# Kernel optimization log

Measured on AMD Instinct MI355X. Metric: run time of the kernel, lower is better.

Reference implementation:

```python
import jax, jax.numpy as jnp
import numpy as np

B, H, S, DK, DV = 2, 16, 2048, 64, 64


def setup_inputs() -> dict:
    key = jax.random.key(0)
    kq, kk, kv = jax.random.split(key, 3)
    Q = jax.random.normal(kq, (B, H, S, DK), dtype=jnp.float32)
    K = jax.random.normal(kk, (B, H, S, DK), dtype=jnp.float32)
    V = jax.random.normal(kv, (B, H, S, DV), dtype=jnp.float32)
    # causal mask: True = masked (upper triangle), broadcast to [B,H,S,S]
    causal = jnp.triu(jnp.ones((S, S), dtype=bool), k=1)
    attn_mask = jnp.broadcast_to(causal, (B, H, S, S))
    return {"Q": Q, "K": K, "V": V, "attn_mask": attn_mask}


def reference(Q, K, V, attn_mask):
    d_k = Q.shape[-1]
    # scores: [B,H,len_q,len_k]
    scores = jnp.einsum('bhqd,bhkd->bhqk', Q, K) / jnp.sqrt(jnp.float32(d_k))
    scores = jnp.where(attn_mask, -jnp.inf, scores)
    attn = jax.nn.softmax(scores, axis=-1)
    # context: [B,H,len_q,d_v]
    context = jnp.einsum('bhqk,bhkv->bhqv', attn, V)
    return context
```

## Files before the change

kernel.cpp:

```cpp
#include <hip/hip_runtime.h>
#include <hip/hip_bf16.h>
#include <math.h>

#define S_LEN 2048
#define DKV 64
#define NBH 32
#define QBLK 64
#define NQB (S_LEN / QBLK)
#define NKT (S_LEN / 64)
#define TILE_SH 4096

typedef __attribute__((ext_vector_type(8))) short bf16x8;
typedef __attribute__((ext_vector_type(16))) float f32x16;
typedef __attribute__((ext_vector_type(4))) float f32x4;
typedef __attribute__((ext_vector_type(4))) unsigned uint4v;

__device__ __forceinline__ short f2bf(float f) {
    union { float f; unsigned u; } x; x.f = f;
    unsigned r = (x.u + 0x7FFFu + ((x.u >> 16) & 1u)) >> 16;
    return (short)r;
}

__device__ __forceinline__ unsigned cvtpk(float lo, float hi) {
    unsigned r;
    asm("v_cvt_pk_bf16_f32 %0, %1, %2" : "=v"(r) : "v"(lo), "v"(hi));
    return r;
}

#define GLOAD_LDS16(g, s)                                                        \
    __builtin_amdgcn_global_load_lds(                                            \
        (const __attribute__((address_space(1))) unsigned*)(g),                  \
        (__attribute__((address_space(3))) unsigned*)(s), 16, 0, 0)

__global__ __launch_bounds__(256)
void prep_kv(const float* __restrict__ K, const float* __restrict__ V,
             short* __restrict__ wsK, short* __restrict__ wsV) {
    const int tile = blockIdx.x, bh = blockIdx.y, tid = threadIdx.x;
    const float* Kp = K + ((size_t)bh * S_LEN + tile * 64) * DKV;
    const float* Vp = V + ((size_t)bh * S_LEN + tile * 64) * DKV;
    short* outK = wsK + ((size_t)bh * NKT + tile) * TILE_SH;
    short* outV = wsV + ((size_t)bh * NKT + tile) * TILE_SH;

    __shared__ short Klds[64 * 64];
    __shared__ short Vl[64 * 64];

#pragma unroll
    for (int i = 0; i < 2; ++i) {
        const int chunk = i * 256 + tid;
        const int row = chunk >> 3, c8 = chunk & 7;
        const float* ksrc = Kp + row * DKV + c8 * 8;
        float4 a = *(const float4*)ksrc, b = *(const float4*)(ksrc + 4);
        uint4v tw;
        tw[0] = cvtpk(a.x, a.y); tw[1] = cvtpk(a.z, a.w);
        tw[2] = cvtpk(b.x, b.y); tw[3] = cvtpk(b.z, b.w);
        const int sidxK = (((c8 >> 1) * 2 + (row >> 5)) * 64) |
                          (((c8 & 1) << 5) | (row & 31));
        *(uint4v*)&Klds[sidxK * 8] = tw;

        const float* vs = Vp + row * DKV + c8 * 8;
        float4 c = *(const float4*)vs, d = *(const float4*)(vs + 4);
        uint4v uw;
        uw[0] = cvtpk(c.x, c.y); uw[1] = cvtpk(c.z, c.w);
        uw[2] = cvtpk(d.x, d.y); uw[3] = cvtpk(d.z, d.w);
        *(uint4v*)&Vl[chunk * 8] = uw;
    }
    __syncthreads();

#pragma unroll
    for (int i = 0; i < 2; ++i) {
        const int s = i * 256 + tid;
        *(bf16x8*)(outK + s * 8) = *(const bf16x8*)&Klds[s * 8];
        const int group = s >> 6;
        const int cc = group >> 1, th = group & 1;
        const int lane = s & 63;
        const int hh = lane >> 5, r31 = lane & 31;
        const int vd = 32 * th + r31;
        const int key0 = 16 * cc + 8 * hh;
        bf16x8 t;
#pragma unroll
        for (int j = 0; j < 8; ++j) t[j] = Vl[(key0 + j) * 64 + vd];
        *(bf16x8*)(outV + s * 8) = t;
    }
}

__global__ __launch_bounds__(256, 4)
void attn_fwd(const float* __restrict__ Q, const short* __restrict__ wsK,
              const short* __restrict__ wsV, float* __restrict__ O) {
    const int tid = threadIdx.x;
    const int l   = tid & 63;
    const int w   = tid >> 6;
    const int st  = w & 1;
    const int ks  = w >> 1;
    const int h   = l >> 5;
    const int q31 = l & 31;

    const int id = blockIdx.x;
    const int bh = ((id & 7) << 2) | ((id >> 3) & 3);
    const int r  = (id >> 5) & 7;
    const int qt = id >> 8;
    const int qb = (qt == 0) ? (31 - r) : (qt == 1) ? r
                 : (qt == 2) ? (23 - r) : (8 + r);

    __shared__ char smem[32768];
    char* kls = smem + ks * 16384;
    float* combp = (float*)smem;

    const float SCALE = 0.125f * 1.4426950408889634f;
    const float M0 = 12.0f;

    const int qrow = qb * QBLK + st * 32 + q31;

    bf16x8 qf[4];
    {
        const float* qr = Q + ((size_t)bh * S_LEN + qrow) * DKV;
#pragma unroll
        for (int c = 0; c < 4; ++c) {
            const int k0 = c * 16 + h * 8;
            float4 f0 = *(const float4*)(qr + k0);
            float4 f1 = *(const float4*)(qr + k0 + 4);
            bf16x8 t;
            t[0] = f2bf(f0.x * SCALE); t[1] = f2bf(f0.y * SCALE);
            t[2] = f2bf(f0.z * SCALE); t[3] = f2bf(f0.w * SCALE);
            t[4] = f2bf(f1.x * SCALE); t[5] = f2bf(f1.y * SCALE);
            t[6] = f2bf(f1.z * SCALE); t[7] = f2bf(f1.w * SCALE);
            qf[c] = t;
        }
    }

    const char* gK = (const char*)(wsK + (size_t)bh * NKT * TILE_SH);
    const char* gV = (const char*)(wsV + (size_t)bh * NKT * TILE_SH);
    const int lb = l * 16;

    float lsum = 0.0f;
    f32x16 oacc[2];
#pragma unroll
    for (int vh = 0; vh < 2; ++vh)
#pragma unroll
        for (int rr = 0; rr < 16; ++rr) oacc[vh][rr] = 0.0f;

    if (ks <= qb) {
        const char* kT = gK + (size_t)ks * 8192;
#pragma unroll
        for (int i = 0; i < 4; ++i)
            GLOAD_LDS16(kT + st * 4096 + i * 1024 + lb,
                        kls + st * 4096 + i * 1024);
    }

    const int niter = qb / 2 + 1;
    int cur = 0;
    for (int it = 0; it < niter; ++it) {
        const int t = 2 * it + ks;
        const bool active = (t <= qb);

        asm volatile("s_waitcnt vmcnt(0)" ::: "memory");
        __syncthreads();

        if (active) {
            bf16x8 kf[8];
#pragma unroll
            for (int i = 0; i < 8; ++i)
                kf[i] = *(const bf16x8*)(kls + cur * 8192 + i * 1024 + lb);

            if (t + 2 <= qb) {
                const char* kT2 = gK + (size_t)(t + 2) * 8192;
                char* nb = kls + (cur ^ 1) * 8192;
#pragma unroll
                for (int i = 0; i < 4; ++i)
                    GLOAD_LDS16(kT2 + st * 4096 + i * 1024 + lb,
                                nb + st * 4096 + i * 1024);
            }

            f32x16 sacc[2];
#pragma unroll
            for (int th = 0; th < 2; ++th)
#pragma unroll
                for (int rr = 0; rr < 16; ++rr) sacc[th][rr] = 0.0f;

            __builtin_amdgcn_s_setprio(1);
#pragma unroll
            for (int c = 0; c < 4; ++c)
#pragma unroll
                for (int th = 0; th < 2; ++th)
                    sacc[th] = __builtin_amdgcn_mfma_f32_32x32x16_bf16(
                        kf[c * 2 + th], qf[c], sacc[th], 0, 0, 0);
            __builtin_amdgcn_s_setprio(0);

            const char* vT = gV + (size_t)t * 8192;
            bf16x8 vf[8];
#pragma unroll
            for (int i = 0; i < 8; ++i)
                vf[i] = *(const bf16x8*)(vT + i * 1024 + lb);

            if (t == qb) {
                const int kv0 = t * 64;
#pragma unroll
                for (int th = 0; th < 2; ++th)
#pragma unroll
                    for (int rr = 0; rr < 16; ++rr) {
                        const int key_g = kv0 + 32 * th + (rr & 3) + 8 * (rr >> 2) + 4 * h;
                        if (key_g > qrow) sacc[th][rr] = -3.0e38f;
                    }
            }

            float rs = 0.0f;
            __builtin_amdgcn_s_setprio(1);
#pragma unroll
            for (int c = 0; c < 4; ++c) {
                const int th = c >> 1, cc = c & 1;
                float p8[8];
#pragma unroll
                for (int j = 0; j < 8; ++j) {
                    p8[j] = __builtin_amdgcn_exp2f(sacc[th][8 * cc + j] - M0);
                    rs += p8[j];
                }
                const unsigned W00 = cvtpk(p8[0], p8[1]);
                const unsigned W01 = cvtpk(p8[2], p8[3]);
                const unsigned W10 = cvtpk(p8[4], p8[5]);
                const unsigned W11 = cvtpk(p8[6], p8[7]);
                const unsigned S0 = h ? W00 : W10;
                const unsigned S1 = h ? W01 : W11;
                const unsigned K0 = h ? W10 : W00;
                const unsigned K1 = h ? W11 : W01;
                const unsigned Y0 = __shfl_xor(S0, 32);
                const unsigned Y1 = __shfl_xor(S1, 32);
                uint4v pwv;
                pwv[0] = h ? Y0 : K0;
                pwv[1] = h ? Y1 : K1;
                pwv[2] = h ? K0 : Y0;
                pwv[3] = h ? K1 : Y1;
                const bf16x8 pa = __builtin_bit_cast(bf16x8, pwv);
#pragma unroll
                for (int vh = 0; vh < 2; ++vh)
                    oacc[vh] = __builtin_amdgcn_mfma_f32_32x32x16_bf16(
                        vf[c * 2 + vh], pa, oacc[vh], 0, 0, 0);
            }
            __builtin_amdgcn_s_setprio(0);

            rs += __shfl_xor(rs, 32);
            lsum += rs;
        }
        cur ^= 1;
    }

    __syncthreads();
    if (ks == 1) {
        float* cp = combp + (st * 64 + l) * 33;
        cp[0] = lsum;
#pragma unroll
        for (int vh = 0; vh < 2; ++vh)
#pragma unroll
            for (int rr = 0; rr < 16; ++rr) cp[1 + vh * 16 + rr] = oacc[vh][rr];
    }
    __syncthreads();
    if (ks == 0) {
        const float* cp = combp + (st * 64 + l) * 33;
        const float inv = 1.0f / (lsum + cp[0]);
        float* Op = O + ((size_t)bh * S_LEN + qrow) * DKV;
#pragma unroll
        for (int vh = 0; vh < 2; ++vh) {
#pragma unroll
            for (int g2 = 0; g2 < 4; ++g2) {
                f32x4 ov;
#pragma unroll
                for (int d = 0; d < 4; ++d)
                    ov[d] = (oacc[vh][4 * g2 + d] +
                             cp[1 + vh * 16 + 4 * g2 + d]) * inv;
                *(f32x4*)(Op + 32 * vh + 8 * g2 + 4 * h) = ov;
            }
        }
    }
}

extern "C" void kernel_launch(void* const* d_in, const int* in_sizes, int n_in,
                              void* d_out, int out_size, void* d_ws, size_t ws_size,
                              hipStream_t stream) {
    const float* Q = (const float*)d_in[0];
    const float* K = (const float*)d_in[1];
    const float* V = (const float*)d_in[2];
    float* O = (float*)d_out;

    short* wsK = (short*)d_ws;
    short* wsV = wsK + (size_t)NBH * NKT * TILE_SH;

    dim3 gridp(NKT, NBH);
    prep_kv<<<gridp, 256, 0, stream>>>(K, V, wsK, wsV);
    attn_fwd<<<dim3(NQB * NBH), 256, 0, stream>>>(Q, wsK, wsV, O);
}
```

Before: 47.79 us.

## Double query block to 128 rows and stage V through LDS alongside K

Each workgroup now covers 128 query rows with 512 threads (4 row strips x 2 key splits), so every staged K/V tile serves twice as many queries and the number of workgroups is halved. V tiles, which used to be read straight from global memory, are now copied into LDS together with K by async global-to-LDS loads, and the buffering doubles LDS to 64KB. The grid scheduling order is reworked for 16 query blocks per head. The costs are lower occupancy, a larger LDS footprint, and more wasted masked work on the diagonal tiles.

```diff
diff --git a/kernel.cpp b/kernel.cpp
--- a/kernel.cpp
+++ b/kernel.cpp
@@ -5,7 +5,7 @@
 #define S_LEN 2048
 #define DKV 64
 #define NBH 32
-#define QBLK 64
+#define QBLK 128
 #define NQB (S_LEN / QBLK)
 #define NKT (S_LEN / 64)
 #define TILE_SH 4096
@@ -83,32 +83,31 @@
     }
 }
 
-__global__ __launch_bounds__(256, 4)
+__global__ __launch_bounds__(512, 4)
 void attn_fwd(const float* __restrict__ Q, const short* __restrict__ wsK,
               const short* __restrict__ wsV, float* __restrict__ O) {
     const int tid = threadIdx.x;
     const int l   = tid & 63;
     const int w   = tid >> 6;
-    const int st  = w & 1;
-    const int ks  = w >> 1;
+    const int st  = w & 3;
+    const int ks  = w >> 2;
     const int h   = l >> 5;
     const int q31 = l & 31;
 
-    const int id = blockIdx.x;
-    const int bh = ((id & 7) << 2) | ((id >> 3) & 3);
-    const int r  = (id >> 5) & 7;
-    const int qt = id >> 8;
-    const int qb = (qt == 0) ? (31 - r) : (qt == 1) ? r
-                 : (qt == 2) ? (23 - r) : (8 + r);
-
-    __shared__ char smem[32768];
-    char* kls = smem + ks * 16384;
+    const int id  = blockIdx.x;
+    const int bh  = ((id & 7) << 2) | ((id >> 3) & 3);
+    const int r5  = (id >> 5) & 7;
+    const int qb  = (id < 256) ? (15 - r5) : r5;
+
+    __shared__ char smem[65536];
+    char* stg = smem + ks * 32768;
     float* combp = (float*)smem;
 
     const float SCALE = 0.125f * 1.4426950408889634f;
     const float M0 = 12.0f;
 
     const int qrow = qb * QBLK + st * 32 + q31;
+    const int tmax_st = 2 * qb + (st >> 1);
 
     bf16x8 qf[4];
     {
@@ -138,37 +137,42 @@
 #pragma unroll
         for (int rr = 0; rr < 16; ++rr) oacc[vh][rr] = 0.0f;
 
-    if (ks <= qb) {
-        const char* kT = gK + (size_t)ks * 8192;
+    {
+        const char* src = (st < 2)
+            ? gK + (size_t)ks * 8192 + st * 4096
+            : gV + (size_t)ks * 8192 + (st - 2) * 4096;
+        char* dst = stg + st * 4096;
 #pragma unroll
         for (int i = 0; i < 4; ++i)
-            GLOAD_LDS16(kT + st * 4096 + i * 1024 + lb,
-                        kls + st * 4096 + i * 1024);
-    }
-
-    const int niter = qb / 2 + 1;
+            GLOAD_LDS16(src + i * 1024 + lb, dst + i * 1024);
+    }
+
     int cur = 0;
-    for (int it = 0; it < niter; ++it) {
+    for (int it = 0; it <= qb; ++it) {
         const int t = 2 * it + ks;
-        const bool active = (t <= qb);
 
         asm volatile("s_waitcnt vmcnt(0)" ::: "memory");
         __syncthreads();
 
-        if (active) {
+        if (it < qb) {
+            const int t2 = t + 2;
+            const char* src = (st < 2)
+                ? gK + (size_t)t2 * 8192 + st * 4096
+                : gV + (size_t)t2 * 8192 + (st - 2) * 4096;
+            char* dst = stg + (cur ^ 1) * 16384 + st * 4096;
+#pragma unroll
+            for (int i = 0; i < 4; ++i)
+                GLOAD_LDS16(src + i * 1024 + lb, dst + i * 1024);
+        }
+
+        if (t <= tmax_st) {
+            const char* kb = stg + cur * 16384;
+            const char* vb = kb + 8192;
+
             bf16x8 kf[8];
 #pragma unroll
             for (int i = 0; i < 8; ++i)
-                kf[i] = *(const bf16x8*)(kls + cur * 8192 + i * 1024 + lb);
-
-            if (t + 2 <= qb) {
-                const char* kT2 = gK + (size_t)(t + 2) * 8192;
-                char* nb = kls + (cur ^ 1) * 8192;
-#pragma unroll
-                for (int i = 0; i < 4; ++i)
-                    GLOAD_LDS16(kT2 + st * 4096 + i * 1024 + lb,
-                                nb + st * 4096 + i * 1024);
-            }
+                kf[i] = *(const bf16x8*)(kb + i * 1024 + lb);
 
             f32x16 sacc[2];
 #pragma unroll
@@ -185,13 +189,12 @@
                         kf[c * 2 + th], qf[c], sacc[th], 0, 0, 0);
             __builtin_amdgcn_s_setprio(0);
 
-            const char* vT = gV + (size_t)t * 8192;
             bf16x8 vf[8];
 #pragma unroll
             for (int i = 0; i < 8; ++i)
-                vf[i] = *(const bf16x8*)(vT + i * 1024 + lb);
-
-            if (t == qb) {
+                vf[i] = *(const bf16x8*)(vb + i * 1024 + lb);
+
+            if (t == tmax_st) {
                 const int kv0 = t * 64;
 #pragma unroll
                 for (int th = 0; th < 2; ++th)
@@ -284,5 +287,5 @@
 
     dim3 gridp(NKT, NBH);
     prep_kv<<<gridp, 256, 0, stream>>>(K, V, wsK, wsV);
-    attn_fwd<<<dim3(NQB * NBH), 256, 0, stream>>>(Q, wsK, wsV, O);
-}
+    attn_fwd<<<dim3(NQB * NBH), 512, 0, stream>>>(Q, wsK, wsV, O);
+}
```

Result: slower. 50.18 us (+5.0%).
